# Performance work log

Measured on AMD Instinct MI355X. Metric: run time of the kernel, lower is better.

Reference implementation:

```python
import jax, jax.numpy as jnp
import numpy as np


def _conv_same(x, w, b):
    # 3x3 same-padding conv, NCHW / OIHW (matches ConvNdWithSamePadding with
    # kernel=3, stride=1, dilation=1 -> symmetric pad of 1)
    y = jax.lax.conv_general_dilated(
        x, w, window_strides=(1, 1), padding='SAME',
        dimension_numbers=('NCHW', 'OIHW', 'NCHW'))
    return y + b[None, :, None, None]


def setup_inputs() -> dict:
    key = jax.random.key(0)
    ks = jax.random.split(key, 5)
    B, A, C, H, W = 8, 6, 256, 32, 32
    x = jax.random.normal(ks[0], (B, A, C, H, W), dtype=jnp.float32)
    w_ih = jax.random.normal(ks[1], (3 * C, 2 * C, 3, 3), dtype=jnp.float32) * 0.02
    w_hh = jax.random.normal(ks[2], (3 * C, C, 3, 3), dtype=jnp.float32) * 0.02
    b_ih = jax.random.normal(ks[3], (3 * C,), dtype=jnp.float32) * 0.02
    b_hh = jax.random.normal(ks[4], (3 * C,), dtype=jnp.float32) * 0.02
    return {'x': x, 'w_ih': w_ih, 'w_hh': w_hh, 'b_ih': b_ih, 'b_hh': b_hh,
            'num_iters': 3}


def reference(x, w_ih, w_hh, b_ih, b_hh, num_iters):
    # x: [B, A, C, H, W] per-agent BEV features.
    # Each GNN iteration: message = mean of other agents' features,
    # GRU input = concat(own, message) [2C ch], hidden = own feature [C ch],
    # new feature = ConvGRU cell output.
    B, A, C, H, W = x.shape
    for _ in range(num_iters):
        # mean over the other A-1 agents, computed via total sum (vectorized)
        msg = (jnp.sum(x, axis=1, keepdims=True) - x) / (A - 1)
        inp = jnp.concatenate([x, msg], axis=2).reshape(B * A, 2 * C, H, W)
        h = x.reshape(B * A, C, H, W)
        gi = _conv_same(inp, w_ih, b_ih)   # [B*A, 3C, H, W]
        gh = _conv_same(h, w_hh, b_hh)     # [B*A, 3C, H, W]
        i_r, i_i, i_n = jnp.split(gi, 3, axis=1)
        h_r, h_i, h_n = jnp.split(gh, 3, axis=1)
        resetgate = jax.nn.sigmoid(i_r + h_r)
        inputgate = jax.nn.sigmoid(i_i + h_i)
        newgate = jnp.tanh(i_n + resetgate * h_n)
        hy = newgate + inputgate * (h - newgate)
        x = hy.reshape(B, A, C, H, W)
    return x
```

## Files before the change

### kernel.cpp

```cpp
#include <hip/hip_runtime.h>
#include <stdint.h>

typedef unsigned short u16;
typedef __attribute__((ext_vector_type(8))) short short8;
typedef __attribute__((ext_vector_type(4))) float f32x4;

__device__ __forceinline__ u16 f2bf(float f) {
  uint32_t u = __builtin_bit_cast(uint32_t, f);
  u += 0x7fffu + ((u >> 16) & 1u);
  return (u16)(u >> 16);
}

__device__ __forceinline__ void gld16(const void* g, void* l) {
  __builtin_amdgcn_global_load_lds(
      (const __attribute__((address_space(1))) void*)g,
      (__attribute__((address_space(3))) void*)l, 16, 0, 0);
}

__device__ __forceinline__ void waitv(int n) {
  switch (n) {
    case 0: asm volatile("s_waitcnt vmcnt(0)" ::: "memory"); break;
    case 1: asm volatile("s_waitcnt vmcnt(1)" ::: "memory"); break;
    case 2: asm volatile("s_waitcnt vmcnt(2)" ::: "memory"); break;
    case 3: asm volatile("s_waitcnt vmcnt(3)" ::: "memory"); break;
    case 4: asm volatile("s_waitcnt vmcnt(4)" ::: "memory"); break;
    case 5: asm volatile("s_waitcnt vmcnt(5)" ::: "memory"); break;
    default: asm volatile("s_waitcnt vmcnt(6)" ::: "memory"); break;
  }
}

__global__ __launch_bounds__(256) void k_wprep(const float* __restrict__ w_ih,
                                               const float* __restrict__ w_hh,
                                               u16* __restrict__ wA,
                                               u16* __restrict__ wS) {
  const int NA = 8*9*8*192*32;
  const int NS = 8*9*8*96*32;
  for (int idx = blockIdx.x*blockDim.x + threadIdx.x; idx < NA + NS;
       idx += gridDim.x*blockDim.x) {
    if (idx < NA) {
      int kk = idx & 31; int t = idx >> 5;
      int nl = t % 192; t /= 192;
      int kb = t & 7; t >>= 3;
      int tap = t % 9; int cb = t / 9;
      int qq = nl / 96; int rr = nl % 96;
      int g = rr >> 4, cl = rr & 15;
      int c = cb*32 + qq*16 + cl, ci = kb*32 + kk;
      float v;
      if (g < 3) {
        int o = g*256 + c;
        v = w_ih[(o*512 + ci)*9 + tap] - 0.2f * w_ih[(o*512 + 256 + ci)*9 + tap];
      } else {
        int o = (g-3)*256 + c;
        v = w_hh[(o*256 + ci)*9 + tap];
      }
      wA[idx] = f2bf(v);
    } else {
      int j = idx - NA;
      int kk = j & 31; int t = j >> 5;
      int nl = t % 96; t /= 96;
      int kb = t & 7; t >>= 3;
      int tap = t % 9; int cb = t / 9;
      int o = cb*96 + nl, ci = kb*32 + kk;
      wS[j] = f2bf(0.2f * w_ih[(o*512 + 256 + ci)*9 + tap]);
    }
  }
}

__global__ __launch_bounds__(256) void k_xform(const float* __restrict__ src,
                                               u16* __restrict__ xbf,
                                               u16* __restrict__ sbf) {
  __shared__ float lds[32][33];
  const int t = threadIdx.x;
  const int tx = t & 31, ty = t >> 5;
  const int p0 = blockIdx.x*32, c0 = blockIdx.y*32, b = blockIdx.z;
  const int po = t >> 3, co = (t & 7)*4;
  float ss[4] = {0.f,0.f,0.f,0.f};
  for (int a = 0; a < 6; ++a) {
    const int im = b*6 + a;
    const float* sp = src + ((size_t)im*256 + c0)*1024 + p0;
    #pragma unroll
    for (int k = 0; k < 4; ++k) {
      float v = sp[(size_t)(ty + 8*k)*1024 + tx];
      ss[k] += v;
      lds[ty + 8*k][tx] = v;
    }
    __syncthreads();
    ushort4 pk = make_ushort4(f2bf(lds[co+0][po]), f2bf(lds[co+1][po]),
                              f2bf(lds[co+2][po]), f2bf(lds[co+3][po]));
    *(ushort4*)(xbf + ((size_t)im*1024 + p0+po)*256 + c0 + co) = pk;
    __syncthreads();
  }
  #pragma unroll
  for (int k = 0; k < 4; ++k) lds[ty + 8*k][tx] = ss[k];
  __syncthreads();
  ushort4 pk = make_ushort4(f2bf(lds[co+0][po]), f2bf(lds[co+1][po]),
                            f2bf(lds[co+2][po]), f2bf(lds[co+3][po]));
  *(ushort4*)(sbf + ((size_t)b*1024 + p0+po)*256 + c0 + co) = pk;
}

template<int NQ, bool GATES>
__global__ __launch_bounds__(512, 4)
void k_conv(const u16* __restrict__ xin, const u16* __restrict__ wpre,
            float* __restrict__ gsbuf,
            const float* __restrict__ b_ih, const float* __restrict__ b_hh,
            const float* __restrict__ h_in, float* __restrict__ h_out) {
  constexpr int NT    = 512;
  constexpr int RB    = 8 / NQ;
  constexpr int MTC   = 32 / RB;
  constexpr int SLABR = RB + 2;
  constexpr int SLAB  = SLABR*32*32;
  constexpr int NBLK  = NQ*96;
  constexpr int BN    = NBLK*32;
  constexpr int TOTA  = SLABR*128;
  constexpr int TOTB  = BN/8;
  __shared__ __align__(16) u16 slab[2][SLAB];
  __shared__ __align__(16) u16 bbuf[3][BN];

  const int tid = threadIdx.x;
  const int l  = tid & 63;
  const int w  = tid >> 6;
  const int lx = l & 15;
  const int lk = l >> 4;
  const int rg = w / NQ;
  const int q  = w % NQ;

  int bid = blockIdx.x;
  const int cb = bid & 7;
  const int rest = bid >> 3;
  const int mt = rest % MTC;
  const int img = rest / MTC;
  const int h0 = mt * RB;

  const u16* srcimg = xin + (size_t)img * (1024*256);

  const int trf = __builtin_amdgcn_readfirstlane(tid);
  const int myB = TOTB/NT + ((trf < (TOTB % NT)) ? 1 : 0);
  const int myA = TOTA/NT + ((trf < (TOTA % NT)) ? 1 : 0);

  auto stageA = [&](int kb, int sbuf) {
    #pragma unroll
    for (int ii = 0; ii < (TOTA + NT - 1)/NT; ++ii) {
      int i = ii*NT + tid;
      if (i < TOTA) {
        int p = i >> 2, ck = i & 3;
        int pr = p >> 5, pc = p & 31;
        int gr = h0 - 1 + pr;
        gr = gr < 0 ? 0 : (gr > 31 ? 31 : gr);
        int sck = ck ^ ((p >> 1) & 3);
        gld16(srcimg + (gr*32 + pc)*256 + kb*32 + sck*8, &slab[sbuf][i*8]);
      }
    }
  };
  auto stageB = [&](int kb, int tap, int bb) {
    const u16* wb = wpre + (size_t)((cb*9 + tap)*8 + kb) * BN;
    #pragma unroll
    for (int ii = 0; ii < (TOTB + NT - 1)/NT; ++ii) {
      int i = ii*NT + tid;
      if (i < TOTB) {
        int nl = i >> 2, ck = i & 3;
        int sck = ck ^ ((nl >> 1) & 3);
        gld16(wb + nl*32 + sck*8, &bbuf[bb][i*8]);
      }
    }
  };

  f32x4 acc[2][6];
  #pragma unroll
  for (int mi = 0; mi < 2; ++mi)
    #pragma unroll
    for (int g = 0; g < 6; ++g) acc[mi][g] = (f32x4){0.f,0.f,0.f,0.f};

  stageA(0, 0);
  stageB(0, 0, 0);
  stageB(0, 1, 1);

  for (int kb = 0; kb < 8; ++kb) {
    const int sb = kb & 1;
    #pragma unroll
    for (int tap = 0; tap < 9; ++tap) {
      const int tau = kb*9 + tap;
      if (tau == 71) waitv(0);
      else if (tap == 7 && kb < 7) waitv(myA + myB);
      else waitv(myB);
      __builtin_amdgcn_s_barrier();
      __builtin_amdgcn_sched_barrier(0);

      if (tap == 6 && kb < 7) stageA(kb+1, sb^1);
      if (tau <= 69) stageB((tau+2)/9, (tau+2)%9, (tau+2)%3);

      const int dy = tap/3, dx = tap%3;
      const int grow = h0 + rg + dy - 1;
      const bool rowok = (grow >= 0) && (grow < 32);
      const int sr = rg + dy;
      short8 a[2];
      #pragma unroll
      for (int mi = 0; mi < 2; ++mi) {
        const int cc = mi*16 + lx + dx - 1;
        const bool ok = rowok && (cc >= 0) && (cc < 32);
        const int ccc = cc < 0 ? 0 : (cc > 31 ? 31 : cc);
        short8 av = *(const short8*)&slab[sb][(sr*32 + ccc)*32 + (lk ^ ((ccc >> 1) & 3))*8];
        if (!ok) av = (short8){0,0,0,0,0,0,0,0};
        a[mi] = av;
      }
      const u16* bp = &bbuf[tau % 3][(q*96 + lx)*32 + (lk ^ ((lx >> 1) & 3))*8];
      __builtin_amdgcn_s_setprio(1);
      #pragma unroll
      for (int g = 0; g < 6; ++g) {
        short8 bv = *(const short8*)(bp + g*512);
        acc[0][g] = __builtin_amdgcn_mfma_f32_16x16x32_bf16(a[0], bv, acc[0][g], 0, 0, 0);
        acc[1][g] = __builtin_amdgcn_mfma_f32_16x16x32_bf16(a[1], bv, acc[1][g], 0, 0, 0);
      }
      __builtin_amdgcn_s_setprio(0);
    }
  }

  if constexpr (GATES) {
    const int b = img / 6;
    const int c = cb*32 + q*16 + lx;
    const float bir = b_ih[c],  bii = b_ih[256+c], bin_ = b_ih[512+c];
    const float bhr = b_hh[c],  bhi = b_hh[256+c], bhn  = b_hh[512+c];
    const float* gs0 = gsbuf + ((size_t)(b*3+0)*256 + c)*1024;
    const float* gs1 = gsbuf + ((size_t)(b*3+1)*256 + c)*1024;
    const float* gs2 = gsbuf + ((size_t)(b*3+2)*256 + c)*1024;
    const float* hp  = h_in  + ((size_t)img*256 + c)*1024;
    float*       op  = h_out + ((size_t)img*256 + c)*1024;
    const int R = h0 + rg;
    #pragma unroll
    for (int mi = 0; mi < 2; ++mi) {
      const int pix = R*32 + mi*16 + lk*4;
      float4 v0 = *(const float4*)(gs0 + pix);
      float4 v1 = *(const float4*)(gs1 + pix);
      float4 v2 = *(const float4*)(gs2 + pix);
      float4 hv = *(const float4*)(hp + pix);
      float4 o;
      #pragma unroll
      for (int r = 0; r < 4; ++r) {
        float ir  = acc[mi][0][r] + (&v0.x)[r] + bir;
        float ii  = acc[mi][1][r] + (&v1.x)[r] + bii;
        float inn = acc[mi][2][r] + (&v2.x)[r] + bin_;
        float hr  = acc[mi][3][r] + bhr;
        float hi2 = acc[mi][4][r] + bhi;
        float hn  = acc[mi][5][r] + bhn;
        float rgt = 1.f/(1.f + __expf(-(ir+hr)));
        float igt = 1.f/(1.f + __expf(-(ii+hi2)));
        float nx = inn + rgt*hn;
        nx = nx > 20.f ? 20.f : (nx < -20.f ? -20.f : nx);
        float e2 = __expf(-2.f*nx);
        float ng = (1.f - e2)/(1.f + e2);
        (&o.x)[r] = ng + igt*((&hv.x)[r] - ng);
      }
      *(float4*)(op + pix) = o;
    }
  } else {
    const int R = h0 + rg;
    #pragma unroll
    for (int g = 0; g < 6; ++g) {
      const int n = cb*NBLK + q*96 + g*16 + lx;
      float* gp = gsbuf + ((size_t)img*768 + n)*1024;
      #pragma unroll
      for (int mi = 0; mi < 2; ++mi) {
        const int pix = R*32 + mi*16 + lk*4;
        *(float4*)(gp + pix) = make_float4(acc[mi][g][0], acc[mi][g][1],
                                           acc[mi][g][2], acc[mi][g][3]);
      }
    }
  }
}

extern "C" void kernel_launch(void* const* d_in, const int* in_sizes, int n_in,
                              void* d_out, int out_size, void* d_ws, size_t ws_size,
                              hipStream_t stream) {
  const float* x    = (const float*)d_in[0];
  const float* w_ih = (const float*)d_in[1];
  const float* w_hh = (const float*)d_in[2];
  const float* b_ih = (const float*)d_in[3];
  const float* b_hh = (const float*)d_in[4];
  float* out = (float*)d_out;

  char* ws = (char*)d_ws;
  float* m0  = (float*)(ws);
  u16*  xbf  = (u16*)(ws + 50331648);
  u16*  sbf  = (u16*)(ws + 75497472);
  float* gsb = (float*)(ws + 79691776);
  u16*  wA   = (u16*)(ws + 104857600);
  u16*  wS   = (u16*)(ws + 111935488);

  k_wprep<<<2048, 256, 0, stream>>>(w_ih, w_hh, wA, wS);

  for (int it = 0; it < 3; ++it) {
    const float* src = (it == 0) ? x : (it == 1 ? out : m0);
    float* dst = (it == 1) ? m0 : out;
    k_xform<<<dim3(32, 8, 8), 256, 0, stream>>>(src, xbf, sbf);
    k_conv<1, false><<<256, 512, 0, stream>>>(sbf, wS, gsb,
                                              nullptr, nullptr, nullptr, nullptr);
    k_conv<2, true><<<3072, 512, 0, stream>>>(xbf, wA, gsb,
                                              b_ih, b_hh, src, dst);
  }
}
```

Baseline: 1.318 ms.

## Load conv weights directly into registers and shrink blocks to 256 threads

The conv kernel no longer stages weight tiles through a triple-buffered LDS ring. Each lane now loads its B fragments straight from global memory into registers, double-buffered and prefetched one tap ahead, so only the activation slab stays in LDS. Blocks shrink to 4 waves of 4 rows each, the grid doubles, and synchronisation drops to one drain plus barrier per input-channel block instead of one per tap. The trade is more redundant global and L2 reads of weights, since they are no longer shared across waves through LDS, and more VGPR pressure from the register buffers.

New measurement: 2.144 ms. +62.7%, slower.

```diff
diff --git a/kernel.cpp b/kernel.cpp
--- a/kernel.cpp
+++ b/kernel.cpp
@@ -17,16 +17,8 @@
       (__attribute__((address_space(3))) void*)l, 16, 0, 0);
 }
 
-__device__ __forceinline__ void waitv(int n) {
-  switch (n) {
-    case 0: asm volatile("s_waitcnt vmcnt(0)" ::: "memory"); break;
-    case 1: asm volatile("s_waitcnt vmcnt(1)" ::: "memory"); break;
-    case 2: asm volatile("s_waitcnt vmcnt(2)" ::: "memory"); break;
-    case 3: asm volatile("s_waitcnt vmcnt(3)" ::: "memory"); break;
-    case 4: asm volatile("s_waitcnt vmcnt(4)" ::: "memory"); break;
-    case 5: asm volatile("s_waitcnt vmcnt(5)" ::: "memory"); break;
-    default: asm volatile("s_waitcnt vmcnt(6)" ::: "memory"); break;
-  }
+__device__ __forceinline__ void drain() {
+  asm volatile("s_waitcnt vmcnt(0)" ::: "memory");
 }
 
 __global__ __launch_bounds__(256) void k_wprep(const float* __restrict__ w_ih,
@@ -98,69 +90,63 @@
   *(ushort4*)(sbf + ((size_t)b*1024 + p0+po)*256 + c0 + co) = pk;
 }
 
-template<int NQ, bool GATES>
-__global__ __launch_bounds__(512, 4)
+template<bool GATES>
+__global__ __launch_bounds__(256, 3)
 void k_conv(const u16* __restrict__ xin, const u16* __restrict__ wpre,
             float* __restrict__ gsbuf,
             const float* __restrict__ b_ih, const float* __restrict__ b_hh,
             const float* __restrict__ h_in, float* __restrict__ h_out) {
-  constexpr int NT    = 512;
-  constexpr int RB    = 8 / NQ;
-  constexpr int MTC   = 32 / RB;
-  constexpr int SLABR = RB + 2;
-  constexpr int SLAB  = SLABR*32*32;
-  constexpr int NBLK  = NQ*96;
-  constexpr int BN    = NBLK*32;
-  constexpr int TOTA  = SLABR*128;
-  constexpr int TOTB  = BN/8;
+  constexpr int BNROW = GATES ? 192 : 96;
+  constexpr int BN    = BNROW * 32;
+  constexpr int SLAB  = 6*32*32;
+  constexpr int TOTA  = 6*128;
   __shared__ __align__(16) u16 slab[2][SLAB];
-  __shared__ __align__(16) u16 bbuf[3][BN];
 
   const int tid = threadIdx.x;
-  const int l  = tid & 63;
-  const int w  = tid >> 6;
-  const int lx = l & 15;
-  const int lk = l >> 4;
-  const int rg = w / NQ;
-  const int q  = w % NQ;
-
-  int bid = blockIdx.x;
-  const int cb = bid & 7;
-  const int rest = bid >> 3;
-  const int mt = rest % MTC;
-  const int img = rest / MTC;
-  const int h0 = mt * RB;
+  const int l   = tid & 63;
+  const int rg  = tid >> 6;
+  const int lx  = l & 15;
+  const int lk  = l >> 4;
+
+  int cb, q, rest;
+  if constexpr (GATES) {
+    const int nsl = blockIdx.x & 15;
+    cb = nsl & 7; q = nsl >> 3; rest = blockIdx.x >> 4;
+  } else {
+    cb = blockIdx.x & 7; q = 0; rest = blockIdx.x >> 3;
+  }
+  const int mt  = rest & 7;
+  const int img = rest >> 3;
+  const int h0  = mt * 4;
 
   const u16* srcimg = xin + (size_t)img * (1024*256);
-
-  const int trf = __builtin_amdgcn_readfirstlane(tid);
-  const int myB = TOTB/NT + ((trf < (TOTB % NT)) ? 1 : 0);
-  const int myA = TOTA/NT + ((trf < (TOTA % NT)) ? 1 : 0);
+  const u16* wlane = wpre + (q*96 + lx)*32 + lk*8;
 
   auto stageA = [&](int kb, int sbuf) {
     #pragma unroll
-    for (int ii = 0; ii < (TOTA + NT - 1)/NT; ++ii) {
-      int i = ii*NT + tid;
-      if (i < TOTA) {
-        int p = i >> 2, ck = i & 3;
-        int pr = p >> 5, pc = p & 31;
-        int gr = h0 - 1 + pr;
-        gr = gr < 0 ? 0 : (gr > 31 ? 31 : gr);
-        int sck = ck ^ ((p >> 1) & 3);
-        gld16(srcimg + (gr*32 + pc)*256 + kb*32 + sck*8, &slab[sbuf][i*8]);
-      }
+    for (int ii = 0; ii < 3; ++ii) {
+      int i = ii*256 + tid;
+      int p = i >> 2, ck = i & 3;
+      int pr = p >> 5, pc = p & 31;
+      int gr = h0 - 1 + pr;
+      gr = gr < 0 ? 0 : (gr > 31 ? 31 : gr);
+      int sck = ck ^ ((p >> 1) & 3);
+      gld16(srcimg + (gr*32 + pc)*256 + kb*32 + sck*8, &slab[sbuf][i*8]);
     }
   };
-  auto stageB = [&](int kb, int tap, int bb) {
-    const u16* wb = wpre + (size_t)((cb*9 + tap)*8 + kb) * BN;
-    #pragma unroll
-    for (int ii = 0; ii < (TOTB + NT - 1)/NT; ++ii) {
-      int i = ii*NT + tid;
-      if (i < TOTB) {
-        int nl = i >> 2, ck = i & 3;
-        int sck = ck ^ ((nl >> 1) & 3);
-        gld16(wb + nl*32 + sck*8, &bbuf[bb][i*8]);
-      }
+
+  auto loadA = [&](short8 (&a)[2], int DY, int DX, int ssel) {
+    const int grow = h0 + rg + DY - 1;
+    const bool rowok = (grow >= 0) && (grow < 32);
+    const int sr = rg + DY;
+    #pragma unroll
+    for (int mi = 0; mi < 2; ++mi) {
+      const int cc = mi*16 + lx + DX - 1;
+      const bool ok = rowok && (cc >= 0) && (cc < 32);
+      const int ccc = cc < 0 ? 0 : (cc > 31 ? 31 : cc);
+      short8 av = *(const short8*)&slab[ssel][(sr*32 + ccc)*32 + (lk ^ ((ccc >> 1) & 3))*8];
+      if (!ok) av = (short8){0,0,0,0,0,0,0,0};
+      a[mi] = av;
     }
   };
 
@@ -170,58 +156,63 @@
     #pragma unroll
     for (int g = 0; g < 6; ++g) acc[mi][g] = (f32x4){0.f,0.f,0.f,0.f};
 
+  short8 b[2][6];
+
   stageA(0, 0);
-  stageB(0, 0, 0);
-  stageB(0, 1, 1);
-
-  for (int kb = 0; kb < 8; ++kb) {
-    const int sb = kb & 1;
-    #pragma unroll
-    for (int tap = 0; tap < 9; ++tap) {
-      const int tau = kb*9 + tap;
-      if (tau == 71) waitv(0);
-      else if (tap == 7 && kb < 7) waitv(myA + myB);
-      else waitv(myB);
-      __builtin_amdgcn_s_barrier();
-      __builtin_amdgcn_sched_barrier(0);
-
-      if (tap == 6 && kb < 7) stageA(kb+1, sb^1);
-      if (tau <= 69) stageB((tau+2)/9, (tau+2)%9, (tau+2)%3);
-
-      const int dy = tap/3, dx = tap%3;
-      const int grow = h0 + rg + dy - 1;
-      const bool rowok = (grow >= 0) && (grow < 32);
-      const int sr = rg + dy;
-      short8 a[2];
+  drain();
+  {
+    const u16* wb = wlane + (size_t)((cb*9 + 0)*8 + 0) * BN;
+    #pragma unroll
+    for (int g = 0; g < 6; ++g) b[0][g] = *(const short8*)(wb + g*512);
+  }
+  __builtin_amdgcn_s_barrier();
+  __builtin_amdgcn_sched_barrier(0);
+
+  for (int kbp = 0; kbp < 4; ++kbp) {
+    #pragma unroll
+    for (int kb2 = 0; kb2 < 2; ++kb2) {
+      const int kb = kbp*2 + kb2;
+      const int sb = kb2;
       #pragma unroll
-      for (int mi = 0; mi < 2; ++mi) {
-        const int cc = mi*16 + lx + dx - 1;
-        const bool ok = rowok && (cc >= 0) && (cc < 32);
-        const int ccc = cc < 0 ? 0 : (cc > 31 ? 31 : cc);
-        short8 av = *(const short8*)&slab[sb][(sr*32 + ccc)*32 + (lk ^ ((ccc >> 1) & 3))*8];
-        if (!ok) av = (short8){0,0,0,0,0,0,0,0};
-        a[mi] = av;
-      }
-      const u16* bp = &bbuf[tau % 3][(q*96 + lx)*32 + (lk ^ ((lx >> 1) & 3))*8];
-      __builtin_amdgcn_s_setprio(1);
-      #pragma unroll
-      for (int g = 0; g < 6; ++g) {
-        short8 bv = *(const short8*)(bp + g*512);
-        acc[0][g] = __builtin_amdgcn_mfma_f32_16x16x32_bf16(a[0], bv, acc[0][g], 0, 0, 0);
-        acc[1][g] = __builtin_amdgcn_mfma_f32_16x16x32_bf16(a[1], bv, acc[1][g], 0, 0, 0);
-      }
-      __builtin_amdgcn_s_setprio(0);
+      for (int tap = 0; tap < 9; ++tap) {
+        const int cur = (kb2 + tap) & 1;
+        const int nxt = cur ^ 1;
+
+        if (!(kb == 7 && tap == 8)) {
+          const int nkb  = (tap < 8) ? kb : kb + 1;
+          const int ntap = (tap < 8) ? tap + 1 : 0;
+          const u16* wb = wlane + (size_t)((cb*9 + ntap)*8 + nkb) * BN;
+          #pragma unroll
+          for (int g = 0; g < 6; ++g) b[nxt][g] = *(const short8*)(wb + g*512);
+        }
+        if (tap == 6 && kb < 7) stageA(kb+1, sb^1);
+        short8 a[2];
+        loadA(a, tap/3, tap%3, sb);
+        __builtin_amdgcn_s_setprio(1);
+        #pragma unroll
+        for (int g = 0; g < 6; ++g) {
+          acc[0][g] = __builtin_amdgcn_mfma_f32_16x16x32_bf16(a[0], b[cur][g], acc[0][g], 0, 0, 0);
+          acc[1][g] = __builtin_amdgcn_mfma_f32_16x16x32_bf16(a[1], b[cur][g], acc[1][g], 0, 0, 0);
+        }
+        __builtin_amdgcn_s_setprio(0);
+        if (tap == 8) {
+          drain();
+          __builtin_amdgcn_sched_barrier(0);
+          __builtin_amdgcn_s_barrier();
+          __builtin_amdgcn_sched_barrier(0);
+        }
+      }
     }
   }
 
   if constexpr (GATES) {
-    const int b = img / 6;
+    const int bat = img / 6;
     const int c = cb*32 + q*16 + lx;
     const float bir = b_ih[c],  bii = b_ih[256+c], bin_ = b_ih[512+c];
     const float bhr = b_hh[c],  bhi = b_hh[256+c], bhn  = b_hh[512+c];
-    const float* gs0 = gsbuf + ((size_t)(b*3+0)*256 + c)*1024;
-    const float* gs1 = gsbuf + ((size_t)(b*3+1)*256 + c)*1024;
-    const float* gs2 = gsbuf + ((size_t)(b*3+2)*256 + c)*1024;
+    const float* gs0 = gsbuf + ((size_t)(bat*3+0)*256 + c)*1024;
+    const float* gs1 = gsbuf + ((size_t)(bat*3+1)*256 + c)*1024;
+    const float* gs2 = gsbuf + ((size_t)(bat*3+2)*256 + c)*1024;
     const float* hp  = h_in  + ((size_t)img*256 + c)*1024;
     float*       op  = h_out + ((size_t)img*256 + c)*1024;
     const int R = h0 + rg;
@@ -255,7 +246,7 @@
     const int R = h0 + rg;
     #pragma unroll
     for (int g = 0; g < 6; ++g) {
-      const int n = cb*NBLK + q*96 + g*16 + lx;
+      const int n = cb*96 + g*16 + lx;
       float* gp = gsbuf + ((size_t)img*768 + n)*1024;
       #pragma unroll
       for (int mi = 0; mi < 2; ++mi) {
@@ -291,9 +282,9 @@
     const float* src = (it == 0) ? x : (it == 1 ? out : m0);
     float* dst = (it == 1) ? m0 : out;
     k_xform<<<dim3(32, 8, 8), 256, 0, stream>>>(src, xbf, sbf);
-    k_conv<1, false><<<256, 512, 0, stream>>>(sbf, wS, gsb,
-                                              nullptr, nullptr, nullptr, nullptr);
-    k_conv<2, true><<<3072, 512, 0, stream>>>(xbf, wA, gsb,
-                                              b_ih, b_hh, src, dst);
-  }
-}
+    k_conv<false><<<512, 256, 0, stream>>>(sbf, wS, gsb,
+                                           nullptr, nullptr, nullptr, nullptr);
+    k_conv<true><<<6144, 256, 0, stream>>>(xbf, wA, gsb,
+                                           b_ih, b_hh, src, dst);
+  }
+}
```
